# Kernel optimization log

Measured on AMD Instinct MI355X. Metric: run time of the kernel, lower is better.

The kernel has to match this reference:

```python
import jax, jax.numpy as jnp
import numpy as np

D_M, L_OBS, ALPHA, D_H, D_V, N_HEADS = 64, 256, 256, 256, 64, 8


def setup_inputs():
    key = jax.random.key(0)
    ks = jax.random.split(key, 18)
    x_ts = jax.random.normal(ks[0], (D_M, L_OBS), dtype=jnp.float32)
    t_raw = jax.random.uniform(ks[1], (D_M, L_OBS), dtype=jnp.float32) * ALPHA
    drop = jax.random.uniform(ks[2], (D_M, L_OBS)) < 0.5
    t_ts = jnp.where(drop, -1.0, t_raw)  # negative time == invalid observation
    global_means = jax.random.normal(ks[3], (D_M,), dtype=jnp.float32)
    s = 0.05
    return {
        'x_ts': x_ts, 't_ts': t_ts, 'global_means': global_means,
        'conv_w': jax.random.normal(ks[4], (D_H, D_M)) * s,
        'conv_b': jax.random.normal(ks[5], (D_H,)) * s,
        't2v_w': jax.random.normal(ks[6], (N_HEADS, D_V)),
        't2v_phi': jax.random.normal(ks[7], (N_HEADS, D_V)),
        'wq_w': jax.random.normal(ks[8], (N_HEADS, D_V, D_V)) * s,
        'wq_b': jax.random.normal(ks[9], (N_HEADS, D_V)) * s,
        'wk_w': jax.random.normal(ks[10], (N_HEADS, D_V, D_V)) * s,
        'wk_b': jax.random.normal(ks[11], (N_HEADS, D_V)) * s,
        'proj_w': jax.random.normal(ks[12], (D_H, N_HEADS)) * s,
        'proj_b': jax.random.normal(ks[13], (D_H,)) * s,
        'g1_w': jax.random.normal(ks[14], (D_H, 2 * D_H)) * s,
        'g1_b': jax.random.normal(ks[15], (D_H,)) * s,
        'g2_w': jax.random.normal(ks[16], (D_H, D_H)) * s,
        'g2_b': jax.random.normal(ks[17], (D_H,)) * s,
    }


def _time2vec(tau, w, phi):
    # tau [...], w/phi [H, D_V] -> [H, *tau.shape, D_V]; dim 0 linear, rest sin
    shp = (N_HEADS,) + (1,) * tau.ndim + (D_V,)
    full = w.reshape(shp) * tau[None, ..., None] + phi.reshape(shp)
    return jnp.concatenate([full[..., :1], jnp.sin(full[..., 1:])], axis=-1)


def _impute_row(x, t, gm):
    # ALPHA grid via int(time), then forward-fill starting from global mean.
    valid = (~jnp.isnan(x)) & (t >= 0)
    idx = t.astype(jnp.int32)  # truncation matches int(obs_time.item()) for t>=0
    inr = valid & (idx < ALPHA)
    seg = jnp.where(inr, idx, ALPHA)  # invalid obs go to dropped segment
    order = jnp.arange(L_OBS, dtype=jnp.int32)
    last = jax.ops.segment_max(jnp.where(inr, order, -1), seg,
                               num_segments=ALPHA + 1)[:ALPHA]
    present = last >= 0
    vals = x[jnp.clip(last, 0, L_OBS - 1)]          # value written to each slot
    pos = jnp.where(present, jnp.arange(ALPHA, dtype=jnp.int32), -1)
    lastpos = jax.lax.cummax(pos, axis=0)            # last observed slot <= t
    return jnp.where(lastpos >= 0, vals[jnp.clip(lastpos, 0, ALPHA - 1)], gm)


def _forward(x_ts, t_ts, global_means, conv_w, conv_b, t2v_w, t2v_phi,
             wq_w, wq_b, wk_w, wk_b, proj_w, proj_b, g1_w, g1_b, g2_w, g2_b):
    # --- imputation branch ---
    regular = jax.vmap(_impute_row)(x_ts, t_ts, global_means)  # [d_m, alpha]
    e_imp = (conv_w @ regular).T + conv_b                      # [alpha, d_h]
    # --- mTAND branch (masked attention over ragged observations) ---
    valid = (~jnp.isnan(x_ts)) & (t_ts >= 0)                   # [d_m, L]
    x_safe = jnp.where(valid, x_ts, 0.0)
    t_safe = jnp.where(valid, t_ts, 0.0)
    alpha_pts = jnp.arange(ALPHA, dtype=jnp.float32)
    theta_a = _time2vec(alpha_pts, t2v_w, t2v_phi)             # [H, alpha, d_v]
    q = jnp.einsum('had,hed->hae', theta_a, wq_w) + wq_b[:, None, :]
    theta_o = _time2vec(t_safe, t2v_w, t2v_phi)                # [H, d_m, L, d_v]
    k = jnp.einsum('hjld,hed->hjle', theta_o, wk_w) + wk_b[:, None, None, :]
    scores = jnp.einsum('hae,hjle->hjal', q, k) / np.float32(np.sqrt(D_V))
    scores = jnp.where(valid[None, :, None, :], scores, -1e9)  # exp underflows to 0
    attn = jax.nn.softmax(scores, axis=-1)                     # [H, d_m, alpha, L]
    # fully-invalid features: uniform attn * x_safe==0 -> zeros (matches torch)
    interp = jnp.einsum('hjal,jl->jah', attn, x_safe)          # [d_m, alpha, H]
    e_attn = (interp @ proj_w.T + proj_b).mean(axis=0)         # [alpha, d_h]
    # --- hidden_space gate ---
    concat = jnp.concatenate([e_imp, e_attn], axis=-1)         # [alpha, 2*d_h]
    g = jax.nn.sigmoid(jax.nn.relu(concat @ g1_w.T + g1_b) @ g2_w.T + g2_b)
    return g * e_imp + (1.0 - g) * e_attn                      # [alpha, d_h]


def reference(x_ts, t_ts, global_means, conv_w, conv_b, t2v_w, t2v_phi,
              wq_w, wq_b, wk_w, wk_b, proj_w, proj_b, g1_w, g1_b, g2_w, g2_b):
    return _forward(x_ts, t_ts, global_means, conv_w, conv_b, t2v_w, t2v_phi,
                    wq_w, wq_b, wk_w, wk_b, proj_w, proj_b, g1_w, g1_b, g2_w, g2_b)
```

## Files before the change

### kernel.cpp

```cpp
#include <hip/hip_runtime.h>

#define D_M     64
#define L_OBS   256
#define ALPHA   256
#define D_H     256
#define D_V     64
#define N_HEADS 8

typedef _Float16 half8 __attribute__((ext_vector_type(8)));
typedef float    f32x4 __attribute__((ext_vector_type(4)));

__global__ __launch_bounds__(256) void prep_kernel(
    const float* __restrict__ x_ts, const float* __restrict__ t_ts,
    const float* __restrict__ gm,
    const float* __restrict__ t2v_w, const float* __restrict__ t2v_phi,
    const float* __restrict__ wq_w, const float* __restrict__ wq_b,
    const float* __restrict__ wk_w,
    float* __restrict__ regular, float* __restrict__ QWbuf,
    float* __restrict__ QWabsG)
{
    const int tid = threadIdx.x;

    __shared__ int   last[ALPHA];
    __shared__ float vals[ALPHA];
    __shared__ int   wtot[4];
    __shared__ __align__(16) float wq_s[D_V][68];
    __shared__ __align__(16) float thA[16][68];
    __shared__ __align__(16) float QaT[16][68];

    if (blockIdx.x < D_M) {
        const int m  = blockIdx.x;
        const int l  = tid;
        const int wv = tid >> 6;
        const int ln = tid & 63;
        last[l] = -1;
        __syncthreads();
        float x = x_ts[m * L_OBS + l];
        float t = t_ts[m * L_OBS + l];
        bool valid = (x == x) && (t >= 0.0f);
        int idx = (int)t;
        if (valid && idx < ALPHA) atomicMax(&last[idx], l);
        __syncthreads();
        int li = last[l];
        vals[l] = (li >= 0) ? x_ts[m * L_OBS + li] : 0.0f;
        int p = (li >= 0) ? l : -1;
        #pragma unroll
        for (int s = 1; s < 64; s <<= 1) {
            int q = __shfl_up(p, s);
            if (ln >= s && q > p) p = q;
        }
        if (ln == 63) wtot[wv] = p;
        __syncthreads();
        int pre = -1;
        for (int w = 0; w < 4; w++)
            if (w < wv && wtot[w] > pre) pre = wtot[w];
        int lp = (pre > p) ? pre : p;
        regular[m * ALPHA + l] = (lp >= 0) ? vals[lp] : gm[m];
    } else {
        const int pb = blockIdx.x - D_M;
        const int h  = pb >> 4;
        const int a0 = (pb & 15) * 16;

        {
            const float4* w4 = (const float4*)(wq_w + h * D_V * D_V);
            #pragma unroll
            for (int i = 0; i < 4; i++) {
                int f = i * 256 + tid;
                float4 v = w4[f];
                int e = f >> 4, c = (f & 15) * 4;
                *(float4*)&wq_s[e][c] = v;
            }
        }
        {
            int al = tid >> 4, j0 = (tid & 15) * 4;
            float tv = (float)(a0 + al);
            #pragma unroll
            for (int j = 0; j < 4; j++) {
                int d = j0 + j;
                float f = t2v_w[h * D_V + d] * tv + t2v_phi[h * D_V + d];
                thA[al][d] = (d == 0) ? f : __sinf(f);
            }
        }
        __syncthreads();

        {
            const int e  = tid >> 2;
            const int ap = tid & 3;
            float accA[4] = {0.f, 0.f, 0.f, 0.f};
            const float4* wrow = (const float4*)&wq_s[e][0];
            #pragma unroll
            for (int j = 0; j < 16; j++) {
                float4 w = wrow[j];
                #pragma unroll
                for (int k = 0; k < 4; k++) {
                    float4 tv = *(const float4*)&thA[ap + 4 * k][j * 4];
                    accA[k] += w.x * tv.x + w.y * tv.y + w.z * tv.z + w.w * tv.w;
                }
            }
            float bq = wq_b[h * D_V + e];
            #pragma unroll
            for (int k = 0; k < 4; k++) QaT[ap + 4 * k][e] = accA[k] + bq;
        }
        __syncthreads();

        const int d  = tid >> 2;
        const int ap = tid & 3;
        float accB[4] = {0.f, 0.f, 0.f, 0.f};
        #pragma unroll 4
        for (int e4 = 0; e4 < 16; e4++) {
            const float* wkp = &wk_w[(h * D_V + e4 * 4) * D_V + d];
            float w0 = wkp[0];
            float w1 = wkp[D_V];
            float w2 = wkp[2 * D_V];
            float w3 = wkp[3 * D_V];
            #pragma unroll
            for (int k = 0; k < 4; k++) {
                float4 qv = *(const float4*)&QaT[ap + 4 * k][e4 * 4];
                accB[k] += qv.x * w0 + qv.y * w1 + qv.z * w2 + qv.w * w3;
            }
        }
        #pragma unroll
        for (int k = 0; k < 4; k++)
            QWbuf[h * D_V * ALPHA + d * ALPHA + a0 + ap + 4 * k] = accB[k];

        __syncthreads();
        #pragma unroll
        for (int k = 0; k < 4; k++)
            wq_s[d][ap + 4 * k] = (d == 0) ? 0.0f : fabsf(accB[k]);
        __syncthreads();
        if (tid < 16) {
            float s = 0.0f;
            #pragma unroll 8
            for (int dd = 0; dd < D_V; dd++) s += wq_s[dd][tid];
            QWabsG[h * ALPHA + a0 + tid] = s;
        }
    }
}

__global__ __launch_bounds__(256) void attn_mfma_kernel(
    const float* __restrict__ x_ts, const float* __restrict__ t_ts,
    const float* __restrict__ t2v_w, const float* __restrict__ t2v_phi,
    const float* __restrict__ QWbuf, const float* __restrict__ QWabsG,
    float* __restrict__ interp)
{
    const int m   = blockIdx.x;
    const int h   = blockIdx.y;
    const int tid = threadIdx.x;
    const int wv  = tid >> 6;
    const int ln  = tid & 63;
    const int lg  = ln >> 4;
    const int lc  = ln & 15;

    __shared__ float t_sh[L_OBS], x_sh[L_OBS], mk_sh[L_OBS];
    __shared__ float w_sh[D_V], phi_sh[D_V];
    __shared__ __align__(16) _Float16 hiB[1024];
    __shared__ __align__(16) _Float16 reB[1024];
    __shared__ float red_s[8];

    {
        float x = x_ts[m * L_OBS + tid];
        float t = t_ts[m * L_OBS + tid];
        bool v = (x == x) && (t >= 0.0f);
        x_sh[tid]  = v ? x : 0.0f;
        t_sh[tid]  = v ? t : 0.0f;
        mk_sh[tid] = v ? 0.0f : -1.0e9f;
        float tmx = v ? t : -3.0e38f;
        float tmn = v ? t : 3.0e38f;
        #pragma unroll
        for (int s = 1; s < 64; s <<= 1) {
            tmx = fmaxf(tmx, __shfl_xor(tmx, s));
            tmn = fminf(tmn, __shfl_xor(tmn, s));
        }
        if (ln == 0) { red_s[wv] = tmx; red_s[4 + wv] = tmn; }
    }
    if (tid < D_V)          w_sh[tid]         = t2v_w[h * D_V + tid];
    else if (tid < 2 * D_V) phi_sh[tid - D_V] = t2v_phi[h * D_V + tid - D_V];
    __syncthreads();

    const float tmaxv = fmaxf(fmaxf(red_s[0], red_s[1]), fmaxf(red_s[2], red_s[3]));
    const float tminv = fminf(fminf(red_s[4], red_s[5]), fminf(red_s[6], red_s[7]));
    const bool  anyv  = tmaxv > -1.0e37f;

    const float* __restrict__ QWh = QWbuf + h * D_V * ALPHA;
    const float w0 = w_sh[0], p0 = phi_sh[0];
    const float SCALE2 = 0.18033688011112042f;

    half8 ahf[4][2], arf[4][2];
    float qw0[4][4], sB[4][4];
    #pragma unroll
    for (int at = 0; at < 4; at++) {
        const int abase = wv * 64 + at * 16;
        const int arowA = abase + lc;
        #pragma unroll
        for (int kb = 0; kb < 2; kb++) {
            #pragma unroll
            for (int j = 0; j < 8; j++) {
                int d = 1 + kb * 32 + ((j >> 2) << 4) + (lg << 2) + (j & 3);
                float q = (d < D_V) ? QWh[d * ALPHA + arowA] : 0.0f;
                _Float16 qh = (_Float16)q;
                ahf[at][kb][j] = qh;
                arf[at][kb][j] = (_Float16)(q - (float)qh);
            }
        }
        const int arowD = abase + lg * 4;
        #pragma unroll
        for (int r = 0; r < 4; r++) {
            float q0 = QWh[arowD + r];
            qw0[at][r] = q0;
            float u = q0 * w0;
            float lin = q0 * p0 + fmaxf(u * tmaxv, u * tminv);
            sB[at][r] = SCALE2 * (lin + QWabsG[h * ALPHA + arowD + r]);
        }
    }

    float ssum[4][4], axs[4][4];
    #pragma unroll
    for (int at = 0; at < 4; at++)
        #pragma unroll
        for (int r = 0; r < 4; r++) { ssum[at][r] = 0.0f; axs[at][r] = 0.0f; }

    const int wc  = tid >> 5;
    const int lcw = (tid >> 1) & 15;
    const int dB  = 1 + (wc >> 2) * 32 + (wc & 3) * 4 + ((tid & 1) << 4);

    for (int lt = 0; lt < 16; lt++) {
        if (lt) __syncthreads();
        {
            float tvw = t_sh[lt * 16 + lcw];
            float s0 = __sinf(fmaf(w_sh[(dB + 0) & 63], tvw, phi_sh[(dB + 0) & 63]));
            float s1 = __sinf(fmaf(w_sh[(dB + 1) & 63], tvw, phi_sh[(dB + 1) & 63]));
            float s2 = __sinf(fmaf(w_sh[(dB + 2) & 63], tvw, phi_sh[(dB + 2) & 63]));
            float s3 = __sinf(fmaf(w_sh[(dB + 3) & 63], tvw, phi_sh[(dB + 3) & 63]));
            union { _Float16 hv[4]; float2 f2; } hw, rw;
            hw.hv[0] = (_Float16)s0; hw.hv[1] = (_Float16)s1;
            hw.hv[2] = (_Float16)s2; hw.hv[3] = (_Float16)s3;
            rw.hv[0] = (_Float16)(s0 - (float)hw.hv[0]);
            rw.hv[1] = (_Float16)(s1 - (float)hw.hv[1]);
            rw.hv[2] = (_Float16)(s2 - (float)hw.hv[2]);
            rw.hv[3] = (_Float16)(s3 - (float)hw.hv[3]);
            *(float2*)&hiB[tid * 4] = hw.f2;
            *(float2*)&reB[tid * 4] = rw.f2;
        }
        __syncthreads();
        const int l = lt * 16 + lc;
        const float tv  = t_sh[l];
        const float xv  = x_sh[l];
        const float mkv = mk_sh[l];
        const float tau = fmaf(w0, tv, p0);

        half8 bh[2], br[2];
        #pragma unroll
        for (int kb = 0; kb < 2; kb++) {
            int fi = ((kb * 4 + lg) * 16 + lc) * 8;
            bh[kb] = *(const half8*)&hiB[fi];
            br[kb] = *(const half8*)&reB[fi];
        }

        #pragma unroll
        for (int at = 0; at < 4; at++) {
            f32x4 acc;
            #pragma unroll
            for (int r = 0; r < 4; r++) acc[r] = qw0[at][r] * tau;
            #pragma unroll
            for (int kb = 0; kb < 2; kb++) {
                acc = __builtin_amdgcn_mfma_f32_16x16x32_f16(ahf[at][kb], bh[kb], acc, 0, 0, 0);
                acc = __builtin_amdgcn_mfma_f32_16x16x32_f16(ahf[at][kb], br[kb], acc, 0, 0, 0);
                acc = __builtin_amdgcn_mfma_f32_16x16x32_f16(arf[at][kb], bh[kb], acc, 0, 0, 0);
            }
            #pragma unroll
            for (int r = 0; r < 4; r++) {
                float p = __builtin_amdgcn_exp2f(fmaf(acc[r], SCALE2, mkv) - sB[at][r]);
                ssum[at][r] += p;
                axs[at][r]   = fmaf(p, xv, axs[at][r]);
            }
        }
    }

    #pragma unroll
    for (int at = 0; at < 4; at++) {
        #pragma unroll
        for (int r = 0; r < 4; r++) {
            float S = ssum[at][r];
            float A = axs[at][r];
            S += __shfl_xor(S, 1); A += __shfl_xor(A, 1);
            S += __shfl_xor(S, 2); A += __shfl_xor(A, 2);
            S += __shfl_xor(S, 4); A += __shfl_xor(A, 4);
            S += __shfl_xor(S, 8); A += __shfl_xor(A, 8);
            if (lc == 0) {
                int a = wv * 64 + at * 16 + lg * 4 + r;
                interp[a * (D_M * N_HEADS) + m * N_HEADS + h] =
                    anyv ? (A / S) : 0.0f;
            }
        }
    }
}

__global__ __launch_bounds__(256) void final_kernel(
    const float* __restrict__ regular, const float* __restrict__ interp,
    const float* __restrict__ conv_w, const float* __restrict__ conv_b,
    const float* __restrict__ proj_w, const float* __restrict__ proj_b,
    const float* __restrict__ g1_w, const float* __restrict__ g1_b,
    const float* __restrict__ g2_w, const float* __restrict__ g2_b,
    float* __restrict__ out)
{
    const int a = blockIdx.x;
    const int tid = threadIdx.x;
    __shared__ float isum_s[N_HEADS];
    __shared__ __align__(16) float col[D_M];
    __shared__ __align__(16) float c_s[2 * D_H];
    __shared__ __align__(16) float h_s[D_H];

    if (tid < 64) {
        const float4* i4 = (const float4*)&interp[a * (D_M * N_HEADS) + tid * 8];
        float4 v0 = i4[0], v1 = i4[1];
        float v[8] = {v0.x, v0.y, v0.z, v0.w, v1.x, v1.y, v1.z, v1.w};
        #pragma unroll
        for (int s = 1; s < 64; s <<= 1) {
            #pragma unroll
            for (int j = 0; j < 8; j++) v[j] += __shfl_xor(v[j], s);
        }
        if (tid == 0) {
            #pragma unroll
            for (int j = 0; j < 8; j++) isum_s[j] = v[j];
        }
    } else if (tid < 128) {
        col[tid - 64] = regular[(tid - 64) * ALPHA + a];
    }
    __syncthreads();

    float vattn;
    {
        const float4* p4 = (const float4*)&proj_w[tid * N_HEADS];
        float4 v0 = p4[0], v1 = p4[1];
        float sum = v0.x * isum_s[0] + v0.y * isum_s[1] + v0.z * isum_s[2]
                  + v0.w * isum_s[3] + v1.x * isum_s[4] + v1.y * isum_s[5]
                  + v1.z * isum_s[6] + v1.w * isum_s[7];
        vattn = proj_b[tid] + sum * (1.0f / 64.0f);
    }
    float vimp;
    {
        const float4* row = (const float4*)&conv_w[tid * D_M];
        const float4* c4  = (const float4*)col;
        float s0 = 0.f, s1 = 0.f, s2 = 0.f, s3 = 0.f;
        #pragma unroll
        for (int i = 0; i < D_M / 4; i++) {
            float4 r = row[i]; float4 c = c4[i];
            s0 += r.x * c.x; s1 += r.y * c.y; s2 += r.z * c.z; s3 += r.w * c.w;
        }
        vimp = conv_b[tid] + ((s0 + s1) + (s2 + s3));
    }
    c_s[tid]       = vimp;
    c_s[D_H + tid] = vattn;
    __syncthreads();

    {
        const float4* grow = (const float4*)&g1_w[tid * 2 * D_H];
        const float4* c4 = (const float4*)c_s;
        float s0 = 0.f, s1 = 0.f, s2 = 0.f, s3 = 0.f;
        #pragma unroll 8
        for (int i = 0; i < (2 * D_H) / 4; i++) {
            float4 g = grow[i]; float4 c = c4[i];
            s0 += g.x * c.x; s1 += g.y * c.y; s2 += g.z * c.z; s3 += g.w * c.w;
        }
        float hid = g1_b[tid] + ((s0 + s1) + (s2 + s3));
        h_s[tid] = fmaxf(hid, 0.0f);
    }
    __syncthreads();
    {
        const float4* grow = (const float4*)&g2_w[tid * D_H];
        const float4* h4 = (const float4*)h_s;
        float s0 = 0.f, s1 = 0.f, s2 = 0.f, s3 = 0.f;
        #pragma unroll 8
        for (int i = 0; i < D_H / 4; i++) {
            float4 g = grow[i]; float4 hh = h4[i];
            s0 += g.x * hh.x; s1 += g.y * hh.y; s2 += g.z * hh.z; s3 += g.w * hh.w;
        }
        float z = g2_b[tid] + ((s0 + s1) + (s2 + s3));
        float gate = 1.0f / (1.0f + __expf(-z));
        out[a * D_H + tid] = gate * vimp + (1.0f - gate) * vattn;
    }
}

extern "C" void kernel_launch(void* const* d_in, const int* in_sizes, int n_in,
                              void* d_out, int out_size, void* d_ws, size_t ws_size,
                              hipStream_t stream)
{
    (void)in_sizes; (void)n_in; (void)out_size; (void)ws_size;

    const float* x_ts    = (const float*)d_in[0];
    const float* t_ts    = (const float*)d_in[1];
    const float* gm      = (const float*)d_in[2];
    const float* conv_w  = (const float*)d_in[3];
    const float* conv_b  = (const float*)d_in[4];
    const float* t2v_w   = (const float*)d_in[5];
    const float* t2v_phi = (const float*)d_in[6];
    const float* wq_w    = (const float*)d_in[7];
    const float* wq_b    = (const float*)d_in[8];
    const float* wk_w    = (const float*)d_in[9];
    const float* proj_w  = (const float*)d_in[11];
    const float* proj_b  = (const float*)d_in[12];
    const float* g1_w    = (const float*)d_in[13];
    const float* g1_b    = (const float*)d_in[14];
    const float* g2_w    = (const float*)d_in[15];
    const float* g2_b    = (const float*)d_in[16];

    float* out = (float*)d_out;

    float* ws      = (float*)d_ws;
    float* regular = ws;
    float* QWbuf   = regular + D_M * ALPHA;
    float* interp  = QWbuf + N_HEADS * D_V * ALPHA;
    float* QWabs   = interp + ALPHA * D_M * N_HEADS;

    prep_kernel<<<D_M + 128, 256, 0, stream>>>(
        x_ts, t_ts, gm, t2v_w, t2v_phi, wq_w, wq_b, wk_w,
        regular, QWbuf, QWabs);
    attn_mfma_kernel<<<dim3(D_M, N_HEADS), 256, 0, stream>>>(
        x_ts, t_ts, t2v_w, t2v_phi, QWbuf, QWabs, interp);
    final_kernel<<<ALPHA, 256, 0, stream>>>(
        regular, interp, conv_w, conv_b, proj_w, proj_b,
        g1_w, g1_b, g2_w, g2_b, out);
}
```

Measured before the change: 60.89 us.

## Double-buffer sin fragments, fold softmax bias into accumulator, batch four rows per final block

The attention kernel now double-buffers the time2vec sine fragments in shared memory, computing the next tile's fragments while the current tile's MFMAs run. This removes one barrier per tile. The per-row softmax max bias is folded into the accumulator's initial value, saving a subtraction in the exp path. The final gating kernel processes four alpha rows per block so each weight row read from global memory is reused four times, cutting weight traffic at the cost of fewer blocks and more registers.

```diff
diff --git a/kernel.cpp b/kernel.cpp
--- a/kernel.cpp
+++ b/kernel.cpp
@@ -153,8 +153,8 @@
 
     __shared__ float t_sh[L_OBS], x_sh[L_OBS], mk_sh[L_OBS];
     __shared__ float w_sh[D_V], phi_sh[D_V];
-    __shared__ __align__(16) _Float16 hiB[1024];
-    __shared__ __align__(16) _Float16 reB[1024];
+    __shared__ __align__(16) _Float16 hiB[2048];
+    __shared__ __align__(16) _Float16 reB[2048];
     __shared__ float red_s[8];
 
     {
@@ -184,9 +184,10 @@
     const float* __restrict__ QWh = QWbuf + h * D_V * ALPHA;
     const float w0 = w_sh[0], p0 = phi_sh[0];
     const float SCALE2 = 0.18033688011112042f;
+    const float INV_S2 = 1.0f / 0.18033688011112042f;
 
     half8 ahf[4][2], arf[4][2];
-    float qw0[4][4], sB[4][4];
+    float qw0[4][4], c0b[4][4];
     #pragma unroll
     for (int at = 0; at < 4; at++) {
         const int abase = wv * 64 + at * 16;
@@ -209,7 +210,7 @@
             qw0[at][r] = q0;
             float u = q0 * w0;
             float lin = q0 * p0 + fmaxf(u * tmaxv, u * tminv);
-            sB[at][r] = SCALE2 * (lin + QWabsG[h * ALPHA + arowD + r]);
+            c0b[at][r] = -(lin + QWabsG[h * ALPHA + arowD + r]);
         }
     }
 
@@ -223,44 +224,49 @@
     const int lcw = (tid >> 1) & 15;
     const int dB  = 1 + (wc >> 2) * 32 + (wc & 3) * 4 + ((tid & 1) << 4);
 
+    auto write_frags = [&](int lt, int buf) {
+        float tvw = t_sh[lt * 16 + lcw];
+        float s0 = __sinf(fmaf(w_sh[(dB + 0) & 63], tvw, phi_sh[(dB + 0) & 63]));
+        float s1 = __sinf(fmaf(w_sh[(dB + 1) & 63], tvw, phi_sh[(dB + 1) & 63]));
+        float s2 = __sinf(fmaf(w_sh[(dB + 2) & 63], tvw, phi_sh[(dB + 2) & 63]));
+        float s3 = __sinf(fmaf(w_sh[(dB + 3) & 63], tvw, phi_sh[(dB + 3) & 63]));
+        union { _Float16 hv[4]; float2 f2; } hw, rw;
+        hw.hv[0] = (_Float16)s0; hw.hv[1] = (_Float16)s1;
+        hw.hv[2] = (_Float16)s2; hw.hv[3] = (_Float16)s3;
+        rw.hv[0] = (_Float16)(s0 - (float)hw.hv[0]);
+        rw.hv[1] = (_Float16)(s1 - (float)hw.hv[1]);
+        rw.hv[2] = (_Float16)(s2 - (float)hw.hv[2]);
+        rw.hv[3] = (_Float16)(s3 - (float)hw.hv[3]);
+        *(float2*)&hiB[buf * 1024 + tid * 4] = hw.f2;
+        *(float2*)&reB[buf * 1024 + tid * 4] = rw.f2;
+    };
+
+    write_frags(0, 0);
+    __syncthreads();
+
     for (int lt = 0; lt < 16; lt++) {
-        if (lt) __syncthreads();
-        {
-            float tvw = t_sh[lt * 16 + lcw];
-            float s0 = __sinf(fmaf(w_sh[(dB + 0) & 63], tvw, phi_sh[(dB + 0) & 63]));
-            float s1 = __sinf(fmaf(w_sh[(dB + 1) & 63], tvw, phi_sh[(dB + 1) & 63]));
-            float s2 = __sinf(fmaf(w_sh[(dB + 2) & 63], tvw, phi_sh[(dB + 2) & 63]));
-            float s3 = __sinf(fmaf(w_sh[(dB + 3) & 63], tvw, phi_sh[(dB + 3) & 63]));
-            union { _Float16 hv[4]; float2 f2; } hw, rw;
-            hw.hv[0] = (_Float16)s0; hw.hv[1] = (_Float16)s1;
-            hw.hv[2] = (_Float16)s2; hw.hv[3] = (_Float16)s3;
-            rw.hv[0] = (_Float16)(s0 - (float)hw.hv[0]);
-            rw.hv[1] = (_Float16)(s1 - (float)hw.hv[1]);
-            rw.hv[2] = (_Float16)(s2 - (float)hw.hv[2]);
-            rw.hv[3] = (_Float16)(s3 - (float)hw.hv[3]);
-            *(float2*)&hiB[tid * 4] = hw.f2;
-            *(float2*)&reB[tid * 4] = rw.f2;
-        }
-        __syncthreads();
+        const int cur = lt & 1;
+        half8 bh[2], br[2];
+        #pragma unroll
+        for (int kb = 0; kb < 2; kb++) {
+            int fi = cur * 1024 + ((kb * 4 + lg) * 16 + lc) * 8;
+            bh[kb] = *(const half8*)&hiB[fi];
+            br[kb] = *(const half8*)&reB[fi];
+        }
+        if (lt < 15) write_frags(lt + 1, cur ^ 1);
+
         const int l = lt * 16 + lc;
         const float tv  = t_sh[l];
         const float xv  = x_sh[l];
         const float mkv = mk_sh[l];
         const float tau = fmaf(w0, tv, p0);
 
-        half8 bh[2], br[2];
-        #pragma unroll
-        for (int kb = 0; kb < 2; kb++) {
-            int fi = ((kb * 4 + lg) * 16 + lc) * 8;
-            bh[kb] = *(const half8*)&hiB[fi];
-            br[kb] = *(const half8*)&reB[fi];
-        }
-
         #pragma unroll
         for (int at = 0; at < 4; at++) {
             f32x4 acc;
             #pragma unroll
-            for (int r = 0; r < 4; r++) acc[r] = qw0[at][r] * tau;
+            for (int r = 0; r < 4; r++)
+                acc[r] = fmaf(qw0[at][r], tau, c0b[at][r]);
             #pragma unroll
             for (int kb = 0; kb < 2; kb++) {
                 acc = __builtin_amdgcn_mfma_f32_16x16x32_f16(ahf[at][kb], bh[kb], acc, 0, 0, 0);
@@ -269,12 +275,14 @@
             }
             #pragma unroll
             for (int r = 0; r < 4; r++) {
-                float p = __builtin_amdgcn_exp2f(fmaf(acc[r], SCALE2, mkv) - sB[at][r]);
+                float p = __builtin_amdgcn_exp2f(fmaf(acc[r], SCALE2, mkv));
                 ssum[at][r] += p;
                 axs[at][r]   = fmaf(p, xv, axs[at][r]);
             }
         }
-    }
+        __syncthreads();
+    }
+    (void)INV_S2;
 
     #pragma unroll
     for (int at = 0; at < 4; at++) {
@@ -303,81 +311,108 @@
     const float* __restrict__ g2_w, const float* __restrict__ g2_b,
     float* __restrict__ out)
 {
-    const int a = blockIdx.x;
+    const int a0  = blockIdx.x * 4;
     const int tid = threadIdx.x;
-    __shared__ float isum_s[N_HEADS];
-    __shared__ __align__(16) float col[D_M];
-    __shared__ __align__(16) float c_s[2 * D_H];
-    __shared__ __align__(16) float h_s[D_H];
-
-    if (tid < 64) {
-        const float4* i4 = (const float4*)&interp[a * (D_M * N_HEADS) + tid * 8];
+    __shared__ float isum_s[4][N_HEADS];
+    __shared__ __align__(16) float colT[4][D_M];
+    __shared__ __align__(16) float c_s[4][2 * D_H];
+    __shared__ __align__(16) float h_s[4][D_H];
+
+    {
+        int j = tid >> 6, mm = tid & 63;
+        colT[j][mm] = regular[mm * ALPHA + a0 + j];
+    }
+    {
+        int j = tid >> 6, ln = tid & 63;
+        const float4* i4 = (const float4*)&interp[(a0 + j) * (D_M * N_HEADS) + ln * 8];
         float4 v0 = i4[0], v1 = i4[1];
         float v[8] = {v0.x, v0.y, v0.z, v0.w, v1.x, v1.y, v1.z, v1.w};
         #pragma unroll
         for (int s = 1; s < 64; s <<= 1) {
             #pragma unroll
-            for (int j = 0; j < 8; j++) v[j] += __shfl_xor(v[j], s);
-        }
-        if (tid == 0) {
-            #pragma unroll
-            for (int j = 0; j < 8; j++) isum_s[j] = v[j];
-        }
-    } else if (tid < 128) {
-        col[tid - 64] = regular[(tid - 64) * ALPHA + a];
+            for (int jj = 0; jj < 8; jj++) v[jj] += __shfl_xor(v[jj], s);
+        }
+        if (ln == 0) {
+            #pragma unroll
+            for (int jj = 0; jj < 8; jj++) isum_s[j][jj] = v[jj];
+        }
     }
     __syncthreads();
 
-    float vattn;
+    float vimp[4], vattn[4];
     {
         const float4* p4 = (const float4*)&proj_w[tid * N_HEADS];
-        float4 v0 = p4[0], v1 = p4[1];
-        float sum = v0.x * isum_s[0] + v0.y * isum_s[1] + v0.z * isum_s[2]
-                  + v0.w * isum_s[3] + v1.x * isum_s[4] + v1.y * isum_s[5]
-                  + v1.z * isum_s[6] + v1.w * isum_s[7];
-        vattn = proj_b[tid] + sum * (1.0f / 64.0f);
-    }
-    float vimp;
+        float4 w0 = p4[0], w1 = p4[1];
+        float pb = proj_b[tid];
+        #pragma unroll
+        for (int j = 0; j < 4; j++) {
+            float sum = w0.x * isum_s[j][0] + w0.y * isum_s[j][1]
+                      + w0.z * isum_s[j][2] + w0.w * isum_s[j][3]
+                      + w1.x * isum_s[j][4] + w1.y * isum_s[j][5]
+                      + w1.z * isum_s[j][6] + w1.w * isum_s[j][7];
+            vattn[j] = pb + sum * (1.0f / 64.0f);
+        }
+    }
     {
         const float4* row = (const float4*)&conv_w[tid * D_M];
-        const float4* c4  = (const float4*)col;
-        float s0 = 0.f, s1 = 0.f, s2 = 0.f, s3 = 0.f;
+        float s[4] = {0.f, 0.f, 0.f, 0.f};
         #pragma unroll
         for (int i = 0; i < D_M / 4; i++) {
-            float4 r = row[i]; float4 c = c4[i];
-            s0 += r.x * c.x; s1 += r.y * c.y; s2 += r.z * c.z; s3 += r.w * c.w;
-        }
-        vimp = conv_b[tid] + ((s0 + s1) + (s2 + s3));
-    }
-    c_s[tid]       = vimp;
-    c_s[D_H + tid] = vattn;
+            float4 r = row[i];
+            #pragma unroll
+            for (int j = 0; j < 4; j++) {
+                float4 c = *(const float4*)&colT[j][i * 4];
+                s[j] += r.x * c.x + r.y * c.y + r.z * c.z + r.w * c.w;
+            }
+        }
+        float cb = conv_b[tid];
+        #pragma unroll
+        for (int j = 0; j < 4; j++) vimp[j] = cb + s[j];
+    }
+    #pragma unroll
+    for (int j = 0; j < 4; j++) {
+        c_s[j][tid]       = vimp[j];
+        c_s[j][D_H + tid] = vattn[j];
+    }
     __syncthreads();
 
     {
         const float4* grow = (const float4*)&g1_w[tid * 2 * D_H];
-        const float4* c4 = (const float4*)c_s;
-        float s0 = 0.f, s1 = 0.f, s2 = 0.f, s3 = 0.f;
+        float s[4] = {0.f, 0.f, 0.f, 0.f};
         #pragma unroll 8
         for (int i = 0; i < (2 * D_H) / 4; i++) {
-            float4 g = grow[i]; float4 c = c4[i];
-            s0 += g.x * c.x; s1 += g.y * c.y; s2 += g.z * c.z; s3 += g.w * c.w;
-        }
-        float hid = g1_b[tid] + ((s0 + s1) + (s2 + s3));
-        h_s[tid] = fmaxf(hid, 0.0f);
+            float4 g = grow[i];
+            #pragma unroll
+            for (int j = 0; j < 4; j++) {
+                float4 c = *(const float4*)&c_s[j][i * 4];
+                s[j] += g.x * c.x + g.y * c.y + g.z * c.z + g.w * c.w;
+            }
+        }
+        float gb = g1_b[tid];
+        #pragma unroll
+        for (int j = 0; j < 4; j++) h_s[j][tid] = fmaxf(s[j] + gb, 0.0f);
     }
     __syncthreads();
+
     {
         const float4* grow = (const float4*)&g2_w[tid * D_H];
-        const float4* h4 = (const float4*)h_s;
-        float s0 = 0.f, s1 = 0.f, s2 = 0.f, s3 = 0.f;
+        float s[4] = {0.f, 0.f, 0.f, 0.f};
         #pragma unroll 8
         for (int i = 0; i < D_H / 4; i++) {
-            float4 g = grow[i]; float4 hh = h4[i];
-            s0 += g.x * hh.x; s1 += g.y * hh.y; s2 += g.z * hh.z; s3 += g.w * hh.w;
-        }
-        float z = g2_b[tid] + ((s0 + s1) + (s2 + s3));
-        float gate = 1.0f / (1.0f + __expf(-z));
-        out[a * D_H + tid] = gate * vimp + (1.0f - gate) * vattn;
+            float4 g = grow[i];
+            #pragma unroll
+            for (int j = 0; j < 4; j++) {
+                float4 hh = *(const float4*)&h_s[j][i * 4];
+                s[j] += g.x * hh.x + g.y * hh.y + g.z * hh.z + g.w * hh.w;
+            }
+        }
+        float gb = g2_b[tid];
+        #pragma unroll
+        for (int j = 0; j < 4; j++) {
+            float gate = 1.0f / (1.0f + __expf(-(s[j] + gb)));
+            out[(a0 + j) * D_H + tid] =
+                gate * c_s[j][tid] + (1.0f - gate) * c_s[j][D_H + tid];
+        }
     }
 }
 
@@ -417,7 +452,7 @@
         regular, QWbuf, QWabs);
     attn_mfma_kernel<<<dim3(D_M, N_HEADS), 256, 0, stream>>>(
         x_ts, t_ts, t2v_w, t2v_phi, QWbuf, QWabs, interp);
-    final_kernel<<<ALPHA, 256, 0, stream>>>(
+    final_kernel<<<ALPHA / 4, 256, 0, stream>>>(
         regular, interp, conv_w, conv_b, proj_w, proj_b,
         g1_w, g1_b, g2_w, g2_b, out);
 }
```

New measurement: 60.90 us. About the same (+0.0%).
